# Kernel tuning notes

Measured on AMD Instinct MI355X. Metric: run time of the kernel, lower is better.

Reference implementation:

```python
import jax, jax.numpy as jnp
import numpy as np

B, P, T = 64, 49, 20      # batch, num_pixels (7x7), caption length
V, E, D, A, ENC = 32000, 512, 512, 512, 2048


def setup_inputs() -> dict:
    key = jax.random.key(0)
    ks = jax.random.split(key, 20)
    s = 0.02
    return {
        "features": jax.random.normal(ks[0], (B, P, ENC), jnp.float32),
        "captions": jax.random.randint(ks[1], (B, T), 0, V, jnp.int64),
        "embed_table": jax.random.normal(ks[2], (V, E), jnp.float32) * s,
        "W_ih": jax.random.normal(ks[3], (4 * D, ENC + E), jnp.float32) * s,
        "b_ih": jnp.zeros((4 * D,), jnp.float32),
        "W_hh": jax.random.normal(ks[4], (4 * D, D), jnp.float32) * s,
        "b_hh": jnp.zeros((4 * D,), jnp.float32),
        "W_init_h": jax.random.normal(ks[5], (ENC, D), jnp.float32) * s,
        "b_init_h": jnp.zeros((D,), jnp.float32),
        "W_init_c": jax.random.normal(ks[6], (ENC, D), jnp.float32) * s,
        "b_init_c": jnp.zeros((D,), jnp.float32),
        "W_enc_att": jax.random.normal(ks[7], (ENC, A), jnp.float32) * s,
        "b_enc_att": jnp.zeros((A,), jnp.float32),
        "W_dec_att": jax.random.normal(ks[8], (D, A), jnp.float32) * s,
        "b_dec_att": jnp.zeros((A,), jnp.float32),
        "w_A": jax.random.normal(ks[9], (A,), jnp.float32) * s,
        "b_A": jnp.zeros((), jnp.float32),
        "W_out": jax.random.normal(ks[10], (D, V), jnp.float32) * s,
        "b_out": jnp.zeros((V,), jnp.float32),
    }


def reference(features, captions, embed_table, W_ih, b_ih, W_hh, b_hh,
              W_init_h, b_init_h, W_init_c, b_init_c,
              W_enc_att, b_enc_att, W_dec_att, b_dec_att, w_A, b_A,
              W_out, b_out):
    # Dropout is treated as identity (eval mode) for a deterministic baseline.
    bsz, seq_len = captions.shape
    emb = embed_table[captions]                              # [B,T,E]
    mean_f = features.mean(axis=1)                           # [B,ENC]
    h0 = mean_f @ W_init_h + b_init_h                        # [B,D]
    c0 = mean_f @ W_init_c + b_init_c                        # [B,D]
    enc_states = features @ W_enc_att + b_enc_att            # [B,P,A] (precomputed, loop-invariant)

    def step(carry, x_t):
        h, c = carry
        dec = h @ W_dec_att + b_dec_att                      # [B,A]
        comb = jnp.tanh(enc_states + dec[:, None, :])        # [B,P,A]
        scores = comb @ w_A + b_A                            # [B,P]
        alpha = jax.nn.softmax(scores, axis=1)
        ctx = jnp.einsum('bpe,bp->be', features, alpha)      # [B,ENC]
        x = jnp.concatenate([ctx, x_t], axis=1)              # [B,ENC+E]
        gates = x @ W_ih.T + b_ih + h @ W_hh.T + b_hh        # [B,4D]
        i, f, g, o = jnp.split(gates, 4, axis=1)
        i, f, o = jax.nn.sigmoid(i), jax.nn.sigmoid(f), jax.nn.sigmoid(o)
        g = jnp.tanh(g)
        c2 = f * c + i * g
        h2 = o * jnp.tanh(c2)
        logits = h2 @ W_out + b_out                          # [B,V]
        return (h2, c2), logits

    xs = jnp.swapaxes(emb[:, :seq_len - 1], 0, 1)            # [T-1,B,E]
    _, preds = jax.lax.scan(step, (h0, c0), xs)              # [T-1,B,V]
    preds = jnp.swapaxes(preds, 0, 1)                        # [B,T-1,V]
    vocab = W_out.shape[1]
    last = jnp.zeros((bsz, 1, vocab), preds.dtype)           # t = T-1 never written
    return jnp.concatenate([preds, last], axis=1)            # [B,T,V]
```

## Files before the change

kernel.cpp:

```cpp
#include <hip/hip_runtime.h>

constexpr int B_   = 64;
constexpr int P_   = 49;
constexpr int T_   = 20;
constexpr int V_   = 32000;
constexpr int E_   = 512;
constexpr int D_   = 512;
constexpr int A_   = 512;
constexpr int ENC_ = 2048;
constexpr int NT_  = T_ - 1;
constexpr int KX_  = ENC_ + E_ + D_;
constexpr int KSPL = 8;
constexpr int GCH  = (KX_ / 64) / KSPL;

#define DI __device__ __forceinline__

using u16 = unsigned short;
typedef short   bf16x8 __attribute__((ext_vector_type(8)));
typedef float   f32x4  __attribute__((ext_vector_type(4)));
typedef u16     u16x4  __attribute__((ext_vector_type(4)));

DI float sigm(float x) { return 1.0f / (1.0f + __expf(-x)); }
DI float tanhx(float x) {
  x = fminf(15.0f, fmaxf(-15.0f, x));
  float e = __expf(2.0f * x);
  return (e - 1.0f) / (e + 1.0f);
}
DI u16 f2bf(float x) {
  union { float f; unsigned u; } v{x};
  unsigned r = v.u + 0x7FFF + ((v.u >> 16) & 1);
  return (u16)(r >> 16);
}
DI float bf2f(u16 x) {
  union { unsigned u; float f; } v;
  v.u = ((unsigned)x) << 16;
  return v.f;
}
DI f32x4 mfma16(bf16x8 a, bf16x8 b, f32x4 c) {
  return __builtin_amdgcn_mfma_f32_16x16x32_bf16(a, b, c, 0, 0, 0);
}


__global__ __launch_bounds__(256) void k_mean_bf(const float* __restrict__ feat,
                                                 u16* __restrict__ mfb) {
  int idx = blockIdx.x * 256 + threadIdx.x;
  int b = idx >> 11, e = idx & (ENC_ - 1);
  const float* f = feat + (size_t)b * P_ * ENC_ + e;
  float s = 0.f;
#pragma unroll
  for (int p = 0; p < P_; p++) s += f[(size_t)p * ENC_];
  mfb[idx] = f2bf(s * (1.0f / P_));
}

__global__ __launch_bounds__(256) void k_tr_cvt(const float* __restrict__ in,
    u16* __restrict__ outp, int R, int C) {
  __shared__ float tbuf[32][33];
  int tx = threadIdx.x & 31, ty = threadIdx.x >> 5;
  int c0 = blockIdx.x * 32, r0 = blockIdx.y * 32;
#pragma unroll
  for (int i = 0; i < 4; i++)
    tbuf[ty + 8 * i][tx] = in[(size_t)(r0 + ty + 8 * i) * C + c0 + tx];
  __syncthreads();
#pragma unroll
  for (int i = 0; i < 4; i++)
    outp[(size_t)(c0 + ty + 8 * i) * R + r0 + tx] = f2bf(tbuf[tx][ty + 8 * i]);
}

__global__ __launch_bounds__(256) void k_cvt4(const float* __restrict__ in,
                                              u16* __restrict__ o) {
  int i = blockIdx.x * 256 + threadIdx.x;
  float4 v = ((const float4*)in)[i];
  u16x4 r = {f2bf(v.x), f2bf(v.y), f2bf(v.z), f2bf(v.w)};
  ((u16x4*)o)[i] = r;
}

__global__ __launch_bounds__(256) void k_wg4(const float* __restrict__ Wih,
    const float* __restrict__ Whh, u16* __restrict__ Wg) {
  int i = blockIdx.x * 256 + threadIdx.x;
  int j = i / 768, rem = i - j * 768;
  int k = rem * 4;
  const float* src = (k < ENC_ + E_) ? (Wih + (size_t)j * (ENC_ + E_) + k)
                                     : (Whh + (size_t)j * D_ + (k - ENC_ - E_));
  float4 v = *(const float4*)src;
  u16x4 r = {f2bf(v.x), f2bf(v.y), f2bf(v.z), f2bf(v.w)};
  ((u16x4*)Wg)[i] = r;
}

__global__ __launch_bounds__(256) void k_emb_bf(const int* __restrict__ cap,
    const float* __restrict__ tab, u16* __restrict__ embb) {
  int idx = blockIdx.x * 256 + threadIdx.x;
  int e = idx & (E_ - 1);
  int tb = idx >> 9;
  int b = tb & 63, t = tb >> 6;
  embb[idx] = f2bf(tab[(size_t)cap[b * T_ + t] * E_ + e]);
}

__global__ __launch_bounds__(256) void k_init_bf(const u16* __restrict__ mfb,
    const u16* __restrict__ WiT, const float* __restrict__ binh,
    const float* __restrict__ binc, u16* __restrict__ hbf, float* __restrict__ c) {
  int wid = threadIdx.x >> 6, lane = threadIdx.x & 63;
  int n0 = blockIdx.x * 64 + wid * 16;
  int l16 = lane & 15, lk = lane >> 4;
  const u16* bp = WiT + (size_t)(n0 + l16) * ENC_ + 8 * lk;
  const u16* ap = mfb + (size_t)l16 * ENC_ + 8 * lk;
  f32x4 acc[4] = {};
#pragma unroll 4
  for (int kc = 0; kc < ENC_; kc += 32) {
    bf16x8 b = *(const bf16x8*)(bp + kc);
#pragma unroll
    for (int mf = 0; mf < 4; mf++) {
      bf16x8 a = *(const bf16x8*)(ap + (size_t)mf * 16 * ENC_ + kc);
      acc[mf] = mfma16(a, b, acc[mf]);
    }
  }
  int n = n0 + l16;
#pragma unroll
  for (int mf = 0; mf < 4; mf++) {
    int m = mf * 16 + 4 * lk;
#pragma unroll
    for (int r = 0; r < 4; r++) {
      float v = acc[mf][r];
      if (n < D_) hbf[(size_t)(m + r) * D_ + n] = f2bf(v + binh[n]);
      else        c[(size_t)(m + r) * D_ + (n - D_)] = v + binc[n - D_];
    }
  }
}


__global__ __launch_bounds__(256) void k_enc_bf(const u16* __restrict__ fb,
    const u16* __restrict__ WeT, const float* __restrict__ benc,
    float* __restrict__ encs) {
  int wid = threadIdx.x >> 6, lane = threadIdx.x & 63;
  int m0 = blockIdx.x * 64, n0 = blockIdx.y * 64 + wid * 16;
  int l16 = lane & 15, lk = lane >> 4;
  const u16* ap = fb + (size_t)(m0 + l16) * ENC_ + 8 * lk;
  const u16* bp = WeT + (size_t)(n0 + l16) * ENC_ + 8 * lk;
  f32x4 acc[4] = {};
#pragma unroll 8
  for (int i = 0; i < ENC_ / 32; i++) {
    int kc = i * 32;
    bf16x8 b = *(const bf16x8*)(bp + kc);
#pragma unroll
    for (int mf = 0; mf < 4; mf++) {
      bf16x8 a = *(const bf16x8*)(ap + (size_t)mf * 16 * ENC_ + kc);
      acc[mf] = mfma16(a, b, acc[mf]);
    }
  }
  float bv = benc[n0 + l16];
#pragma unroll
  for (int mf = 0; mf < 4; mf++) {
    int m = m0 + mf * 16 + 4 * lk;
#pragma unroll
    for (int r = 0; r < 4; r++)
      encs[(size_t)(m + r) * A_ + n0 + l16] = acc[mf][r] + bv;
  }
}

__global__ __launch_bounds__(256) void k_gates_bf(const u16* __restrict__ ctxb,
    const u16* __restrict__ embb, const u16* __restrict__ hbf,
    const u16* __restrict__ Wg, float* __restrict__ gp, int t) {
  int wid = threadIdx.x >> 6, lane = threadIdx.x & 63;
  int j0 = blockIdx.x * 64 + wid * 16;
  int sp = blockIdx.y;
  int l16 = lane & 15, lk = lane >> 4;
  const u16* bp = Wg + (size_t)(j0 + l16) * KX_ + 8 * lk;
  f32x4 acc[4] = {};
#pragma unroll
  for (int i = 0; i < KX_ / KSPL / 32; i++) {
    int kc = sp * (KX_ / KSPL) + i * 32;
    int k = kc + 8 * lk;
    bf16x8 b = *(const bf16x8*)(bp + kc);
#pragma unroll
    for (int mf = 0; mf < 4; mf++) {
      int row = mf * 16 + l16;
      const u16* src;
      if (k < ENC_)            src = ctxb + (size_t)row * ENC_ + k;
      else if (k < ENC_ + E_)  src = embb + ((size_t)t * B_ + row) * E_ + (k - ENC_);
      else                     src = hbf + (size_t)row * D_ + (k - ENC_ - E_);
      bf16x8 a = *(const bf16x8*)src;
      acc[mf] = mfma16(a, b, acc[mf]);
    }
  }
#pragma unroll
  for (int mf = 0; mf < 4; mf++) {
    int m = mf * 16 + 4 * lk;
#pragma unroll
    for (int r = 0; r < 4; r++)
      gp[((size_t)sp * B_ + m + r) * (4 * D_) + j0 + l16] = acc[mf][r];
  }
}

__global__ __launch_bounds__(256) void k_logits_all2(const u16* __restrict__ hall,
    const u16* __restrict__ WoT, const float* __restrict__ bout,
    float* __restrict__ out) {
  int wid = threadIdx.x >> 6, lane = threadIdx.x & 63;
  int n0 = blockIdx.x * 64 + wid * 16;
  int l16 = lane & 15, lk = lane >> 4;
  bf16x8 bfr[16];
  const u16* bp = WoT + (size_t)(n0 + l16) * D_ + 8 * lk;
#pragma unroll
  for (int kc = 0; kc < 16; kc++) bfr[kc] = *(const bf16x8*)(bp + kc * 32);
  float bv = bout[n0 + l16];
#pragma unroll 1
  for (int s = 0; s < NT_; s++) {
    const u16* ap = hall + (size_t)s * B_ * D_ + (size_t)l16 * D_ + 8 * lk;
    f32x4 acc[4] = {};
#pragma unroll
    for (int kc = 0; kc < 16; kc++) {
#pragma unroll
      for (int mf = 0; mf < 4; mf++) {
        bf16x8 a = *(const bf16x8*)(ap + (size_t)mf * 16 * D_ + kc * 32);
        acc[mf] = mfma16(a, bfr[kc], acc[mf]);
      }
    }
#pragma unroll
    for (int mf = 0; mf < 4; mf++) {
      int m = mf * 16 + 4 * lk;
#pragma unroll
      for (int r = 0; r < 4; r++)
        out[((size_t)(m + r) * T_ + s) * V_ + n0 + l16] = acc[mf][r] + bv;
    }
  }
#pragma unroll
  for (int mf = 0; mf < 4; mf++) {
    int m = mf * 16 + 4 * lk;
#pragma unroll
    for (int r = 0; r < 4; r++)
      out[((size_t)(m + r) * T_ + (T_ - 1)) * V_ + n0 + l16] = 0.f;
  }
}


__global__ __launch_bounds__(512) void k_att3(const u16* __restrict__ featb,
    const float* __restrict__ encs, const u16* __restrict__ WdT,
    const float* __restrict__ bdec, const float* __restrict__ wA,
    const float* __restrict__ bA, const float* __restrict__ gp,
    const float* __restrict__ bih, const float* __restrict__ bhh,
    const float* __restrict__ c_in, float* __restrict__ c_out,
    u16* __restrict__ hbf, u16* __restrict__ hallp, u16* __restrict__ ctxb,
    int do_reduce, int do_att) {
  __shared__ u16 hsb[D_];
  __shared__ float ds[A_];
  __shared__ float sc[P_];
  __shared__ float inv_s;
  int b = blockIdx.x, y = blockIdx.y, tid = threadIdx.x;

  if (do_reduce) {
    int d = tid;
    float g0 = 0, g1 = 0, g2 = 0, g3 = 0;
#pragma unroll
    for (int s = 0; s < KSPL; s++) {
      const float* g = gp + (size_t)(s * B_ + b) * (4 * D_);
      g0 += g[d]; g1 += g[D_ + d]; g2 += g[2 * D_ + d]; g3 += g[3 * D_ + d];
    }
    g0 += bih[d] + bhh[d];
    g1 += bih[D_ + d] + bhh[D_ + d];
    g2 += bih[2 * D_ + d] + bhh[2 * D_ + d];
    g3 += bih[3 * D_ + d] + bhh[3 * D_ + d];
    float iv = sigm(g0), fv = sigm(g1), gv = tanhx(g2), ov = sigm(g3);
    float cv = fmaf(fv, c_in[b * D_ + d], iv * gv);
    float hv = ov * tanhx(cv);
    u16 hb = f2bf(hv);
    hsb[d] = hb;
    if (y == 0) {
      c_out[b * D_ + d] = cv;
      hbf[b * D_ + d] = hb;
      hallp[b * D_ + d] = hb;
    }
  } else {
    hsb[tid] = hbf[b * D_ + tid];
  }
  __syncthreads();
  if (!do_att) return;

  {
    int w = tid >> 6, lane = tid & 63, l16 = lane & 15, lk = lane >> 4;
#pragma unroll
    for (int f = 0; f < 4; f++) {
      int n = w * 64 + f * 16 + l16;
      const u16* bp = WdT + (size_t)n * D_ + 8 * lk;
      f32x4 acc = {};
#pragma unroll
      for (int kc = 0; kc < D_; kc += 32) {
        bf16x8 av = *(const bf16x8*)(hsb + kc + 8 * lk);
        bf16x8 bv = *(const bf16x8*)(bp + kc);
        acc = mfma16(av, bv, acc);
      }
      if (lk == 0) ds[n] = acc[0] + bdec[n];
    }
  }
  __syncthreads();

  int wv_ = tid >> 6, ln = tid & 63;
  float bA0 = bA[0];
  for (int p = wv_; p < P_; p += 8) {
    const float* ep = encs + (size_t)(b * P_ + p) * A_;
    float s = 0.f;
#pragma unroll
    for (int a = ln; a < A_; a += 64) s += tanhx(ep[a] + ds[a]) * wA[a];
#pragma unroll
    for (int off = 32; off; off >>= 1) s += __shfl_down(s, off);
    if (ln == 0) sc[p] = s + bA0;
  }
  __syncthreads();

  if (tid == 0) {
    float mx = -1e30f;
    for (int p = 0; p < P_; p++) mx = fmaxf(mx, sc[p]);
    float sum = 0.f;
    for (int p = 0; p < P_; p++) { float ex = __expf(sc[p] - mx); sc[p] = ex; sum += ex; }
    inv_s = 1.0f / sum;
  }
  __syncthreads();

  float inv = inv_s;
#pragma unroll
  for (int q = 0; q < 2; q++) {
    int e = y * 1024 + q * 512 + tid;
    const u16* fp = featb + (size_t)b * P_ * ENC_ + e;
    float s = 0.f;
#pragma unroll
    for (int p = 0; p < P_; p++) s = fmaf(bf2f(fp[(size_t)p * ENC_]), sc[p], s);
    ctxb[b * ENC_ + e] = f2bf(s * inv);
  }
}


DI int swz(int row, int slot) { return row * 64 + ((slot ^ (row >> 2)) << 2); }

__global__ __launch_bounds__(256) void k_mean(const float* __restrict__ feat,
                                              float* __restrict__ mf) {
  int idx = blockIdx.x * 256 + threadIdx.x;
  int b = idx >> 11, e = idx & (ENC_ - 1);
  const float* f = feat + (size_t)b * P_ * ENC_ + e;
  float s = 0.f;
#pragma unroll
  for (int p = 0; p < P_; p++) s += f[(size_t)p * ENC_];
  mf[idx] = s * (1.0f / P_);
}

__global__ __launch_bounds__(256) void k_emb(const int* __restrict__ cap,
                                             const float* __restrict__ tab,
                                             float* __restrict__ emb) {
  int idx = blockIdx.x * 256 + threadIdx.x;
  int e  = idx & (E_ - 1);
  int bt = idx >> 9;
  int b = bt / NT_, t = bt - b * NT_;
  int tok = cap[b * T_ + t];
  emb[idx] = tab[(size_t)tok * E_ + e];
}

__global__ __launch_bounds__(256) void k_init(const float* __restrict__ mf,
    const float* __restrict__ Wh, const float* __restrict__ bh,
    const float* __restrict__ Wc, const float* __restrict__ bc,
    float* __restrict__ h, float* __restrict__ c) {
  __shared__ float ms[ENC_];
  int b = blockIdx.y;
  for (int i = threadIdx.x; i < ENC_; i += 256) ms[i] = mf[b * ENC_ + i];
  __syncthreads();
  int d = blockIdx.x * 256 + threadIdx.x;
  const float* W = blockIdx.z ? Wc : Wh;
  float s = (blockIdx.z ? bc : bh)[d];
#pragma unroll 8
  for (int e = 0; e < ENC_; e++) s = fmaf(ms[e], W[(size_t)e * D_ + d], s);
  (blockIdx.z ? c : h)[b * D_ + d] = s;
}

__global__ __launch_bounds__(256) void k_zero_last(float* __restrict__ out) {
  int i = blockIdx.x * 256 + threadIdx.x;
  int b = i / 8000, v4 = i - b * 8000;
  float4 z = {0.f, 0.f, 0.f, 0.f};
  *(float4*)(out + ((size_t)b * T_ + (T_ - 1)) * V_ + (size_t)v4 * 4) = z;
}

__global__ __launch_bounds__(256) void k_enc(const float* __restrict__ Ag,
    const float* __restrict__ Wg, const float* __restrict__ bias,
    float* __restrict__ Cg) {
  __shared__ float As[64 * 64], Ws[64 * 64];
  int m0 = blockIdx.x * 64, n0 = blockIdx.y * 64;
  int tid = threadIdx.x, tn = tid & 15, tm = tid >> 4;
  float acc[4][4] = {};
#pragma unroll 1
  for (int ch = 0; ch < ENC_ / 64; ch++) {
    int k0 = ch * 64;
    __syncthreads();
#pragma unroll
    for (int q = 0; q < 4; q++) {
      int idx = tid + q * 256;
      int row = idx >> 4, slot = idx & 15;
      *(float4*)&As[swz(row, slot)] =
          *(const float4*)(Ag + (size_t)(m0 + row) * ENC_ + k0 + slot * 4);
      *(float4*)&Ws[swz(row, slot)] =
          *(const float4*)(Wg + (size_t)(k0 + row) * A_ + n0 + slot * 4);
    }
    __syncthreads();
#pragma unroll
    for (int kk = 0; kk < 16; kk++) {
      float4 av[4], wv[4];
#pragma unroll
      for (int i = 0; i < 4; i++) av[i] = *(float4*)&As[swz(4 * tm + i, kk)];
#pragma unroll
      for (int u = 0; u < 4; u++) wv[u] = *(float4*)&Ws[swz(4 * kk + u, tn)];
      const float* wq = (const float*)wv;
#pragma unroll
      for (int i = 0; i < 4; i++) {
        const float* aq = (const float*)&av[i];
#pragma unroll
        for (int j = 0; j < 4; j++) {
          float s = acc[i][j];
#pragma unroll
          for (int u = 0; u < 4; u++) s = fmaf(aq[u], wq[u * 4 + j], s);
          acc[i][j] = s;
        }
      }
    }
  }
#pragma unroll
  for (int i = 0; i < 4; i++) {
    int m = m0 + 4 * tm + i, n = n0 + 4 * tn;
    float4 bv = *(const float4*)(bias + n);
    float4 o = {acc[i][0] + bv.x, acc[i][1] + bv.y, acc[i][2] + bv.z, acc[i][3] + bv.w};
    *(float4*)(Cg + (size_t)m * A_ + n) = o;
  }
}

__global__ __launch_bounds__(256) void k_logits(const float* __restrict__ h,
    const float* __restrict__ Wout, const float* __restrict__ bout,
    float* __restrict__ out, int t) {
  __shared__ float As[64 * 64], Ws[64 * 64];
  int n0 = blockIdx.x * 64;
  int tid = threadIdx.x, tn = tid & 15, tm = tid >> 4;
  float acc[4][4] = {};
#pragma unroll 1
  for (int ch = 0; ch < D_ / 64; ch++) {
    int k0 = ch * 64;
    __syncthreads();
#pragma unroll
    for (int q = 0; q < 4; q++) {
      int idx = tid + q * 256;
      int row = idx >> 4, slot = idx & 15;
      *(float4*)&As[swz(row, slot)] =
          *(const float4*)(h + (size_t)row * D_ + k0 + slot * 4);
      *(float4*)&Ws[swz(row, slot)] =
          *(const float4*)(Wout + (size_t)(k0 + row) * V_ + n0 + slot * 4);
    }
    __syncthreads();
#pragma unroll
    for (int kk = 0; kk < 16; kk++) {
      float4 av[4], wv[4];
#pragma unroll
      for (int i = 0; i < 4; i++) av[i] = *(float4*)&As[swz(4 * tm + i, kk)];
#pragma unroll
      for (int u = 0; u < 4; u++) wv[u] = *(float4*)&Ws[swz(4 * kk + u, tn)];
      const float* wq = (const float*)wv;
#pragma unroll
      for (int i = 0; i < 4; i++) {
        const float* aq = (const float*)&av[i];
#pragma unroll
        for (int j = 0; j < 4; j++) {
          float s = acc[i][j];
#pragma unroll
          for (int u = 0; u < 4; u++) s = fmaf(aq[u], wq[u * 4 + j], s);
          acc[i][j] = s;
        }
      }
    }
  }
#pragma unroll
  for (int i = 0; i < 4; i++) {
    int m = 4 * tm + i, n = n0 + 4 * tn;
    float4 bv = *(const float4*)(bout + n);
    float4 o = {acc[i][0] + bv.x, acc[i][1] + bv.y, acc[i][2] + bv.z, acc[i][3] + bv.w};
    *(float4*)(out + ((size_t)m * T_ + t) * V_ + n) = o;
  }
}

__global__ __launch_bounds__(256) void k_gates(const float* __restrict__ ctx,
    const float* __restrict__ emb, const float* __restrict__ h,
    const float* __restrict__ Wih, const float* __restrict__ Whh,
    float* __restrict__ gp, int t) {
  __shared__ float As[64 * 64], Ws[64 * 64];
  int n0 = blockIdx.x * 64;
  int sp = blockIdx.y;
  int tid = threadIdx.x, tn = tid & 15, tm = tid >> 4;
  float acc[4][4] = {};
#pragma unroll 1
  for (int ch = 0; ch < GCH; ch++) {
    int k0 = sp * (GCH * 64) + ch * 64;
    __syncthreads();
#pragma unroll
    for (int q = 0; q < 4; q++) {
      int idx = tid + q * 256;
      int row = idx >> 4, slot = idx & 15;
      int k = k0 + slot * 4;
      float4 xv;
      if (k < ENC_)            xv = *(const float4*)(ctx + (size_t)row * ENC_ + k);
      else if (k < ENC_ + E_)  xv = *(const float4*)(emb + ((size_t)row * NT_ + t) * E_ + (k - ENC_));
      else                     xv = *(const float4*)(h + (size_t)row * D_ + (k - ENC_ - E_));
      *(float4*)&As[swz(row, slot)] = xv;
      int j = n0 + row;
      float4 wv2;
      if (k < ENC_ + E_) wv2 = *(const float4*)(Wih + (size_t)j * (ENC_ + E_) + k);
      else               wv2 = *(const float4*)(Whh + (size_t)j * D_ + (k - ENC_ - E_));
      *(float4*)&Ws[swz(row, slot)] = wv2;
    }
    __syncthreads();
#pragma unroll
    for (int kk = 0; kk < 16; kk++) {
      float4 av[4], wv[4];
#pragma unroll
      for (int i = 0; i < 4; i++) av[i] = *(float4*)&As[swz(4 * tm + i, kk)];
#pragma unroll
      for (int j = 0; j < 4; j++) wv[j] = *(float4*)&Ws[swz(4 * tn + j, kk)];
#pragma unroll
      for (int i = 0; i < 4; i++) {
        const float* aq = (const float*)&av[i];
#pragma unroll
        for (int j = 0; j < 4; j++) {
          const float* wqj = (const float*)&wv[j];
          float s = acc[i][j];
#pragma unroll
          for (int u = 0; u < 4; u++) s = fmaf(aq[u], wqj[u], s);
          acc[i][j] = s;
        }
      }
    }
  }
#pragma unroll
  for (int i = 0; i < 4; i++) {
    int b = 4 * tm + i, j = n0 + 4 * tn;
    float4 o = {acc[i][0], acc[i][1], acc[i][2], acc[i][3]};
    *(float4*)(gp + ((size_t)(sp * B_ + b)) * (4 * D_) + j) = o;
  }
}

__global__ __launch_bounds__(512) void k_att(const float* __restrict__ feat,
    const float* __restrict__ encs, const float* __restrict__ Wdec,
    const float* __restrict__ bdec, const float* __restrict__ wA,
    const float* __restrict__ bA, const float* __restrict__ gp,
    const float* __restrict__ bih, const float* __restrict__ bhh,
    float* __restrict__ h, float* __restrict__ c, float* __restrict__ ctx,
    int do_reduce, int do_att) {
  __shared__ float hs[D_];
  __shared__ float ds[A_];
  __shared__ float sc[P_];
  __shared__ float inv_s;
  int b = blockIdx.x, tid = threadIdx.x;

  if (do_reduce) {
    int d = tid;
    float g0 = 0, g1 = 0, g2 = 0, g3 = 0;
#pragma unroll
    for (int s = 0; s < KSPL; s++) {
      const float* g = gp + (size_t)(s * B_ + b) * (4 * D_);
      g0 += g[d]; g1 += g[D_ + d]; g2 += g[2 * D_ + d]; g3 += g[3 * D_ + d];
    }
    g0 += bih[d] + bhh[d];
    g1 += bih[D_ + d] + bhh[D_ + d];
    g2 += bih[2 * D_ + d] + bhh[2 * D_ + d];
    g3 += bih[3 * D_ + d] + bhh[3 * D_ + d];
    float iv = sigm(g0), fv = sigm(g1), gv = tanhx(g2), ov = sigm(g3);
    float cv = fmaf(fv, c[b * D_ + d], iv * gv);
    float hv = ov * tanhx(cv);
    c[b * D_ + d] = cv;
    h[b * D_ + d] = hv;
    hs[d] = hv;
  } else {
    hs[tid] = h[b * D_ + tid];
  }
  __syncthreads();
  if (!do_att) return;

  {
    int a = tid;
    float s = bdec[a];
#pragma unroll 8
    for (int d = 0; d < D_; d++) s = fmaf(hs[d], Wdec[(size_t)d * A_ + a], s);
    ds[a] = s;
  }
  __syncthreads();

  int wv_ = tid >> 6, ln = tid & 63;
  float bA0 = bA[0];
  for (int p = wv_; p < P_; p += 8) {
    const float* ep = encs + (size_t)(b * P_ + p) * A_;
    float s = 0.f;
#pragma unroll
    for (int a = ln; a < A_; a += 64) s += tanhx(ep[a] + ds[a]) * wA[a];
#pragma unroll
    for (int off = 32; off; off >>= 1) s += __shfl_down(s, off);
    if (ln == 0) sc[p] = s + bA0;
  }
  __syncthreads();

  if (tid == 0) {
    float mx = -1e30f;
    for (int p = 0; p < P_; p++) mx = fmaxf(mx, sc[p]);
    float sum = 0.f;
    for (int p = 0; p < P_; p++) { float ex = __expf(sc[p] - mx); sc[p] = ex; sum += ex; }
    inv_s = 1.0f / sum;
  }
  __syncthreads();

  float inv = inv_s;
  for (int e = tid; e < ENC_; e += 512) {
    const float* fp = feat + (size_t)b * P_ * ENC_ + e;
    float s = 0.f;
#pragma unroll
    for (int p = 0; p < P_; p++) s = fmaf(fp[(size_t)p * ENC_], sc[p], s);
    ctx[b * ENC_ + e] = s * inv;
  }
}


extern "C" void kernel_launch(void* const* d_in, const int* in_sizes, int n_in,
                              void* d_out, int out_size, void* d_ws, size_t ws_size,
                              hipStream_t stream) {
  const float* features = (const float*)d_in[0];
  const int*   captions = (const int*)d_in[1];
  const float* table    = (const float*)d_in[2];
  const float* Wih  = (const float*)d_in[3];
  const float* bih  = (const float*)d_in[4];
  const float* Whh  = (const float*)d_in[5];
  const float* bhh  = (const float*)d_in[6];
  const float* Winh = (const float*)d_in[7];
  const float* binh = (const float*)d_in[8];
  const float* Winc = (const float*)d_in[9];
  const float* binc = (const float*)d_in[10];
  const float* Wenc = (const float*)d_in[11];
  const float* benc = (const float*)d_in[12];
  const float* Wdec = (const float*)d_in[13];
  const float* bdec = (const float*)d_in[14];
  const float* wA   = (const float*)d_in[15];
  const float* bA   = (const float*)d_in[16];
  const float* Wout = (const float*)d_in[17];
  const float* bout = (const float*)d_in[18];
  float* out = (float*)d_out;

  constexpr size_t F_ENC = (size_t)B_ * P_ * A_;
  constexpr size_t F_C   = (size_t)B_ * D_;
  constexpr size_t F_GP  = (size_t)KSPL * B_ * 4 * D_;
  constexpr size_t U_WOT = (size_t)V_ * D_;
  constexpr size_t U_WG  = (size_t)(4 * D_) * KX_;
  constexpr size_t U_HBF = (size_t)B_ * D_;
  constexpr size_t U_CTX = (size_t)B_ * ENC_;
  constexpr size_t U_FEAT = (size_t)B_ * P_ * ENC_;
  constexpr size_t U_WET = (size_t)A_ * ENC_;
  constexpr size_t U_EMB = (size_t)NT_ * B_ * E_;
  constexpr size_t U_WDT = (size_t)A_ * D_;
  constexpr size_t U_HALL = (size_t)NT_ * B_ * D_;
  static_assert(U_EMB + U_WDT <= U_WET, "embb+WdT overlay WeT region");
  constexpr size_t NEED_BYTES =
      (F_ENC + 2 * F_C + F_GP) * 4 +
      (U_WOT + U_WG + U_HBF + U_CTX + U_FEAT + U_WET + U_HALL) * 2;

  if (ws_size >= NEED_BYTES) {
    float* ws = (float*)d_ws;
    float* enc_states = ws;
    float* cbuf0  = enc_states + F_ENC;
    float* cbuf1  = cbuf0 + F_C;
    float* gparts = cbuf1 + F_C;
    u16* WoT   = (u16*)(gparts + F_GP);
    u16* Wg    = WoT + U_WOT;
    u16* hbf   = Wg + U_WG;
    u16* ctxb  = hbf + U_HBF;
    u16* featb = ctxb + U_CTX;
    u16* wetr  = featb + U_FEAT;
    u16* WeT   = wetr;
    u16* embb  = wetr;
    u16* WdT   = wetr + U_EMB;
    u16* hall  = wetr + U_WET;
    u16* WiT   = (u16*)gparts;
    u16* mfb   = ctxb;
    float* cb[2] = {cbuf0, cbuf1};

    k_mean_bf<<<512, 256, 0, stream>>>(features, mfb);
    k_tr_cvt<<<dim3(D_ / 32, ENC_ / 32), 256, 0, stream>>>(Winh, WiT, ENC_, D_);
    k_tr_cvt<<<dim3(D_ / 32, ENC_ / 32), 256, 0, stream>>>(Winc, WiT + (size_t)D_ * ENC_, ENC_, D_);
    k_init_bf<<<16, 256, 0, stream>>>(mfb, WiT, binh, binc, hbf, cbuf0);
    k_cvt4<<<(int)(U_FEAT / 4 / 256), 256, 0, stream>>>(features, featb);
    k_tr_cvt<<<dim3(A_ / 32, ENC_ / 32), 256, 0, stream>>>(Wenc, WeT, ENC_, A_);
    k_enc_bf<<<dim3(49, 8), 256, 0, stream>>>(featb, WeT, benc, enc_states);
    k_emb_bf<<<2432, 256, 0, stream>>>(captions, table, embb);
    k_tr_cvt<<<dim3(A_ / 32, D_ / 32), 256, 0, stream>>>(Wdec, WdT, D_, A_);
    k_tr_cvt<<<dim3(V_ / 32, D_ / 32), 256, 0, stream>>>(Wout, WoT, D_, V_);
    k_wg4<<<(int)(U_WG / 4 / 256), 256, 0, stream>>>(Wih, Whh, Wg);

    for (int t = 0; t < NT_; t++) {
      u16* hallp = (t > 0) ? (hall + (size_t)(t - 1) * B_ * D_) : hall;
      const float* cin = cb[(t > 0 ? (t - 1) : 0) & 1];
      float* cout = cb[t & 1];
      k_att3<<<dim3(64, 2), 512, 0, stream>>>(featb, enc_states, WdT, bdec, wA,
                                              bA, gparts, bih, bhh, cin, cout,
                                              hbf, hallp, ctxb, t > 0 ? 1 : 0, 1);
      k_gates_bf<<<dim3(32, KSPL), 256, 0, stream>>>(ctxb, embb, hbf, Wg, gparts, t);
    }
    k_att3<<<dim3(64, 1), 512, 0, stream>>>(featb, enc_states, WdT, bdec, wA,
                                            bA, gparts, bih, bhh,
                                            cb[(NT_ - 1) & 1], cb[NT_ & 1], hbf,
                                            hall + (size_t)(NT_ - 1) * B_ * D_,
                                            ctxb, 1, 0);
    k_logits_all2<<<500, 256, 0, stream>>>(hall, WoT, bout, out);
  } else {
    float* ws = (float*)d_ws;
    float* enc_states = ws;
    float* mean_f = enc_states + (size_t)B_ * P_ * A_;
    float* emb    = mean_f + (size_t)B_ * ENC_;
    float* h      = emb + (size_t)B_ * NT_ * E_;
    float* c      = h + (size_t)B_ * D_;
    float* ctx    = c + (size_t)B_ * D_;
    float* gparts = ctx + (size_t)B_ * ENC_;

    k_mean<<<512, 256, 0, stream>>>(features, mean_f);
    k_emb<<<2432, 256, 0, stream>>>(captions, table, emb);
    k_init<<<dim3(2, 64, 2), 256, 0, stream>>>(mean_f, Winh, binh, Winc, binc, h, c);
    k_enc<<<dim3(49, 8), 256, 0, stream>>>(features, Wenc, benc, enc_states);
    k_zero_last<<<2000, 256, 0, stream>>>(out);

    for (int t = 0; t < NT_; t++) {
      k_att<<<64, 512, 0, stream>>>(features, enc_states, Wdec, bdec, wA, bA,
                                    gparts, bih, bhh, h, c, ctx, t > 0 ? 1 : 0, 1);
      if (t > 0)
        k_logits<<<500, 256, 0, stream>>>(h, Wout, bout, out, t - 1);
      k_gates<<<dim3(32, KSPL), 256, 0, stream>>>(ctx, emb, h, Wih, Whh, gparts, t);
    }
    k_att<<<64, 512, 0, stream>>>(features, enc_states, Wdec, bdec, wA, bA,
                                  gparts, bih, bhh, h, c, ctx, 1, 0);
    k_logits<<<500, 256, 0, stream>>>(h, Wout, bout, out, NT_ - 1);
  }
}
```

Baseline: 1.264 ms.

## Fuse prologue kernels, per-step embedding gather, and restructure logits GEMM

Merges the many prologue conversion and transpose kernels into one multi-role launch, and merges the init and encoder-projection GEMMs into a second. The per-step attention kernel now gathers that step's embedding, and gate K-splits drop from 8 to 4. The attention grid is no longer split across ctx halves, so each block computes the full context with vectorized loads. The logits kernel is retiled to keep h fragments in registers and stage outputs in shared memory for coalesced float4 stores. This cuts launch count and improves store coalescing, at the cost of less parallelism per step and a very large shared buffer in the fused prologue.

```diff
diff --git a/kernel.cpp b/kernel.cpp
--- a/kernel.cpp
+++ b/kernel.cpp
@@ -12,6 +12,7 @@
 constexpr int KX_  = ENC_ + E_ + D_;
 constexpr int KSPL = 8;
 constexpr int GCH  = (KX_ / 64) / KSPL;
+constexpr int KS4  = 4;
 
 #define DI __device__ __forceinline__
 
@@ -40,23 +41,13 @@
   return __builtin_amdgcn_mfma_f32_16x16x32_bf16(a, b, c, 0, 0, 0);
 }
 
-
-__global__ __launch_bounds__(256) void k_mean_bf(const float* __restrict__ feat,
-                                                 u16* __restrict__ mfb) {
-  int idx = blockIdx.x * 256 + threadIdx.x;
-  int b = idx >> 11, e = idx & (ENC_ - 1);
-  const float* f = feat + (size_t)b * P_ * ENC_ + e;
-  float s = 0.f;
-#pragma unroll
-  for (int p = 0; p < P_; p++) s += f[(size_t)p * ENC_];
-  mfb[idx] = f2bf(s * (1.0f / P_));
-}
-
-__global__ __launch_bounds__(256) void k_tr_cvt(const float* __restrict__ in,
-    u16* __restrict__ outp, int R, int C) {
-  __shared__ float tbuf[32][33];
+constexpr int PRO1_BLOCKS = 18756;
+
+DI void dev_tr_cvt(const float* in, u16* outp, int R, int C, int bx, int by,
+                   char* smem) {
+  float (*tbuf)[33] = (float(*)[33])smem;
   int tx = threadIdx.x & 31, ty = threadIdx.x >> 5;
-  int c0 = blockIdx.x * 32, r0 = blockIdx.y * 32;
+  int c0 = bx * 32, r0 = by * 32;
 #pragma unroll
   for (int i = 0; i < 4; i++)
     tbuf[ty + 8 * i][tx] = in[(size_t)(r0 + ty + 8 * i) * C + c0 + tx];
@@ -66,99 +57,249 @@
     outp[(size_t)(c0 + ty + 8 * i) * R + r0 + tx] = f2bf(tbuf[tx][ty + 8 * i]);
 }
 
-__global__ __launch_bounds__(256) void k_cvt4(const float* __restrict__ in,
-                                              u16* __restrict__ o) {
-  int i = blockIdx.x * 256 + threadIdx.x;
-  float4 v = ((const float4*)in)[i];
-  u16x4 r = {f2bf(v.x), f2bf(v.y), f2bf(v.z), f2bf(v.w)};
-  ((u16x4*)o)[i] = r;
-}
-
-__global__ __launch_bounds__(256) void k_wg4(const float* __restrict__ Wih,
-    const float* __restrict__ Whh, u16* __restrict__ Wg) {
-  int i = blockIdx.x * 256 + threadIdx.x;
-  int j = i / 768, rem = i - j * 768;
-  int k = rem * 4;
-  const float* src = (k < ENC_ + E_) ? (Wih + (size_t)j * (ENC_ + E_) + k)
-                                     : (Whh + (size_t)j * D_ + (k - ENC_ - E_));
-  float4 v = *(const float4*)src;
-  u16x4 r = {f2bf(v.x), f2bf(v.y), f2bf(v.z), f2bf(v.w)};
-  ((u16x4*)Wg)[i] = r;
-}
-
-__global__ __launch_bounds__(256) void k_emb_bf(const int* __restrict__ cap,
-    const float* __restrict__ tab, u16* __restrict__ embb) {
-  int idx = blockIdx.x * 256 + threadIdx.x;
-  int e = idx & (E_ - 1);
-  int tb = idx >> 9;
-  int b = tb & 63, t = tb >> 6;
-  embb[idx] = f2bf(tab[(size_t)cap[b * T_ + t] * E_ + e]);
-}
-
-__global__ __launch_bounds__(256) void k_init_bf(const u16* __restrict__ mfb,
+__global__ __launch_bounds__(256) void k_pro1(
+    const float* __restrict__ feat, const float* __restrict__ Winh,
+    const float* __restrict__ Winc, const float* __restrict__ Wenc,
+    const float* __restrict__ Wdec, const float* __restrict__ Wout,
+    const float* __restrict__ Wih, const float* __restrict__ Whh,
+    float* __restrict__ out, u16* __restrict__ mfb, u16* __restrict__ featb,
+    u16* __restrict__ WiT, u16* __restrict__ WeT, u16* __restrict__ WdT,
+    u16* __restrict__ WoT, u16* __restrict__ Wg) {
+  __shared__ __align__(16) char smem[67584];
+  int bid = blockIdx.x;
+  if (bid < 2000) {
+    int i = bid * 256 + threadIdx.x;
+    int b = i / 8000, v4 = i - b * 8000;
+    float4 z = {0.f, 0.f, 0.f, 0.f};
+    *(float4*)(out + ((size_t)b * T_ + (T_ - 1)) * V_ + (size_t)v4 * 4) = z;
+  } else if (bid < 8272) {
+    int i = (bid - 2000) * 256 + threadIdx.x;
+    float4 v = ((const float4*)feat)[i];
+    u16x4 r = {f2bf(v.x), f2bf(v.y), f2bf(v.z), f2bf(v.w)};
+    ((u16x4*)featb)[i] = r;
+  } else if (bid < 8784) {
+    int idx = (bid - 8272) * 256 + threadIdx.x;
+    int b = idx >> 11, e = idx & (ENC_ - 1);
+    const float* f = feat + (size_t)b * P_ * ENC_ + e;
+    float s = 0.f;
+#pragma unroll
+    for (int p = 0; p < P_; p++) s += f[(size_t)p * ENC_];
+    mfb[idx] = f2bf(s * (1.0f / P_));
+  } else if (bid < 9808) {
+    int l = bid - 8784;
+    dev_tr_cvt(Winh, WiT, ENC_, D_, l & 15, l >> 4, smem);
+  } else if (bid < 10832) {
+    int l = bid - 9808;
+    dev_tr_cvt(Winc, WiT + (size_t)D_ * ENC_, ENC_, D_, l & 15, l >> 4, smem);
+  } else if (bid < 11856) {
+    int l = bid - 10832;
+    dev_tr_cvt(Wenc, WeT, ENC_, A_, l & 15, l >> 4, smem);
+  } else if (bid < 12112) {
+    int l = bid - 11856;
+    dev_tr_cvt(Wdec, WdT, D_, A_, l & 15, l >> 4, smem);
+  } else if (bid < 12612) {
+    int l = bid - 12112;
+    int bx = l % 250, by = l / 250;
+    u16 (*ld)[264] = (u16(*)[264])smem;
+    int v0 = bx * 128, k0 = by * 256;
+    int vf = (threadIdx.x & 31) * 4, kk = threadIdx.x >> 5;
+#pragma unroll 4
+    for (int p = 0; p < 32; p++) {
+      int k = kk + p * 8;
+      float4 v = *(const float4*)(Wout + (size_t)(k0 + k) * V_ + v0 + vf);
+      ld[vf + 0][k] = f2bf(v.x);
+      ld[vf + 1][k] = f2bf(v.y);
+      ld[vf + 2][k] = f2bf(v.z);
+      ld[vf + 3][k] = f2bf(v.w);
+    }
+    __syncthreads();
+    int v = threadIdx.x >> 1, h = threadIdx.x & 1;
+    u16* op = WoT + (size_t)(v0 + v) * D_ + k0 + h * 128;
+#pragma unroll
+    for (int i = 0; i < 16; i++)
+      *(bf16x8*)(op + i * 8) = *(const bf16x8*)(&ld[v][h * 128 + i * 8]);
+  } else {
+    int i = (bid - 12612) * 256 + threadIdx.x;
+    int j = i / 768, rem = i - j * 768;
+    int k = rem * 4;
+    const float* src = (k < ENC_ + E_) ? (Wih + (size_t)j * (ENC_ + E_) + k)
+                                       : (Whh + (size_t)j * D_ + (k - ENC_ - E_));
+    float4 v = *(const float4*)src;
+    u16x4 r = {f2bf(v.x), f2bf(v.y), f2bf(v.z), f2bf(v.w)};
+    ((u16x4*)Wg)[i] = r;
+  }
+}
+
+
+__global__ __launch_bounds__(256) void k_pro2(const u16* __restrict__ mfb,
     const u16* __restrict__ WiT, const float* __restrict__ binh,
-    const float* __restrict__ binc, u16* __restrict__ hbf, float* __restrict__ c) {
-  int wid = threadIdx.x >> 6, lane = threadIdx.x & 63;
-  int n0 = blockIdx.x * 64 + wid * 16;
-  int l16 = lane & 15, lk = lane >> 4;
-  const u16* bp = WiT + (size_t)(n0 + l16) * ENC_ + 8 * lk;
-  const u16* ap = mfb + (size_t)l16 * ENC_ + 8 * lk;
-  f32x4 acc[4] = {};
-#pragma unroll 4
-  for (int kc = 0; kc < ENC_; kc += 32) {
-    bf16x8 b = *(const bf16x8*)(bp + kc);
-#pragma unroll
-    for (int mf = 0; mf < 4; mf++) {
-      bf16x8 a = *(const bf16x8*)(ap + (size_t)mf * 16 * ENC_ + kc);
-      acc[mf] = mfma16(a, b, acc[mf]);
-    }
-  }
-  int n = n0 + l16;
-#pragma unroll
-  for (int mf = 0; mf < 4; mf++) {
-    int m = mf * 16 + 4 * lk;
-#pragma unroll
-    for (int r = 0; r < 4; r++) {
-      float v = acc[mf][r];
-      if (n < D_) hbf[(size_t)(m + r) * D_ + n] = f2bf(v + binh[n]);
-      else        c[(size_t)(m + r) * D_ + (n - D_)] = v + binc[n - D_];
-    }
-  }
-}
-
-
-__global__ __launch_bounds__(256) void k_enc_bf(const u16* __restrict__ fb,
+    const float* __restrict__ binc, u16* __restrict__ hbf,
+    float* __restrict__ c, const u16* __restrict__ featb,
     const u16* __restrict__ WeT, const float* __restrict__ benc,
     float* __restrict__ encs) {
   int wid = threadIdx.x >> 6, lane = threadIdx.x & 63;
-  int m0 = blockIdx.x * 64, n0 = blockIdx.y * 64 + wid * 16;
   int l16 = lane & 15, lk = lane >> 4;
-  const u16* ap = fb + (size_t)(m0 + l16) * ENC_ + 8 * lk;
-  const u16* bp = WeT + (size_t)(n0 + l16) * ENC_ + 8 * lk;
-  f32x4 acc[4] = {};
+  if (blockIdx.x < 16) {
+    int n0 = blockIdx.x * 64 + wid * 16;
+    const u16* bp = WiT + (size_t)(n0 + l16) * ENC_ + 8 * lk;
+    const u16* ap = mfb + (size_t)l16 * ENC_ + 8 * lk;
+    f32x4 acc[4] = {};
+#pragma unroll 4
+    for (int kc = 0; kc < ENC_; kc += 32) {
+      bf16x8 b = *(const bf16x8*)(bp + kc);
+#pragma unroll
+      for (int mf = 0; mf < 4; mf++) {
+        bf16x8 a = *(const bf16x8*)(ap + (size_t)mf * 16 * ENC_ + kc);
+        acc[mf] = mfma16(a, b, acc[mf]);
+      }
+    }
+    int n = n0 + l16;
+#pragma unroll
+    for (int mf = 0; mf < 4; mf++) {
+      int m = mf * 16 + 4 * lk;
+#pragma unroll
+      for (int r = 0; r < 4; r++) {
+        float v = acc[mf][r];
+        if (n < D_) hbf[(size_t)(m + r) * D_ + n] = f2bf(v + binh[n]);
+        else        c[(size_t)(m + r) * D_ + (n - D_)] = v + binc[n - D_];
+      }
+    }
+  } else {
+    int l = blockIdx.x - 16;
+    int m0 = (l % 49) * 64, n0 = (l / 49) * 64 + wid * 16;
+    const u16* ap = featb + (size_t)(m0 + l16) * ENC_ + 8 * lk;
+    const u16* bp = WeT + (size_t)(n0 + l16) * ENC_ + 8 * lk;
+    f32x4 acc[4] = {};
 #pragma unroll 8
-  for (int i = 0; i < ENC_ / 32; i++) {
-    int kc = i * 32;
-    bf16x8 b = *(const bf16x8*)(bp + kc);
+    for (int i = 0; i < ENC_ / 32; i++) {
+      int kc = i * 32;
+      bf16x8 b = *(const bf16x8*)(bp + kc);
+#pragma unroll
+      for (int mf = 0; mf < 4; mf++) {
+        bf16x8 a = *(const bf16x8*)(ap + (size_t)mf * 16 * ENC_ + kc);
+        acc[mf] = mfma16(a, b, acc[mf]);
+      }
+    }
+    float bv = benc[n0 + l16];
 #pragma unroll
     for (int mf = 0; mf < 4; mf++) {
-      bf16x8 a = *(const bf16x8*)(ap + (size_t)mf * 16 * ENC_ + kc);
-      acc[mf] = mfma16(a, b, acc[mf]);
-    }
-  }
-  float bv = benc[n0 + l16];
-#pragma unroll
-  for (int mf = 0; mf < 4; mf++) {
-    int m = m0 + mf * 16 + 4 * lk;
-#pragma unroll
-    for (int r = 0; r < 4; r++)
-      encs[(size_t)(m + r) * A_ + n0 + l16] = acc[mf][r] + bv;
-  }
-}
-
-__global__ __launch_bounds__(256) void k_gates_bf(const u16* __restrict__ ctxb,
-    const u16* __restrict__ embb, const u16* __restrict__ hbf,
-    const u16* __restrict__ Wg, float* __restrict__ gp, int t) {
+      int m = m0 + mf * 16 + 4 * lk;
+#pragma unroll
+      for (int r = 0; r < 4; r++)
+        encs[(size_t)(m + r) * A_ + n0 + l16] = acc[mf][r] + bv;
+    }
+  }
+}
+
+
+__global__ __launch_bounds__(512) void k_att5(const u16* __restrict__ featb,
+    const float* __restrict__ encs, const u16* __restrict__ WdT,
+    const float* __restrict__ bdec, const float* __restrict__ wA,
+    const float* __restrict__ bA, const float* __restrict__ gp,
+    const float* __restrict__ bih, const float* __restrict__ bhh,
+    float* __restrict__ c, u16* __restrict__ hbf, u16* __restrict__ hallp,
+    u16* __restrict__ ctxb, const int* __restrict__ cap,
+    const float* __restrict__ tab, u16* __restrict__ embt, int t,
+    int do_reduce, int do_att) {
+  __shared__ u16 hsb[D_];
+  __shared__ float ds[A_];
+  __shared__ float sc[P_];
+  __shared__ float inv_s;
+  int b = blockIdx.x, tid = threadIdx.x;
+
+  if (do_att) {
+    int tok = cap[b * T_ + t];
+    embt[(size_t)b * E_ + tid] = f2bf(tab[(size_t)tok * E_ + tid]);
+  }
+
+  if (do_reduce) {
+    int d = tid;
+    float g0 = 0, g1 = 0, g2 = 0, g3 = 0;
+#pragma unroll
+    for (int s = 0; s < KS4; s++) {
+      const float* g = gp + (size_t)(s * B_ + b) * (4 * D_);
+      g0 += g[d]; g1 += g[D_ + d]; g2 += g[2 * D_ + d]; g3 += g[3 * D_ + d];
+    }
+    g0 += bih[d] + bhh[d];
+    g1 += bih[D_ + d] + bhh[D_ + d];
+    g2 += bih[2 * D_ + d] + bhh[2 * D_ + d];
+    g3 += bih[3 * D_ + d] + bhh[3 * D_ + d];
+    float iv = sigm(g0), fv = sigm(g1), gv = tanhx(g2), ov = sigm(g3);
+    float cv = fmaf(fv, c[b * D_ + d], iv * gv);
+    float hv = ov * tanhx(cv);
+    c[b * D_ + d] = cv;
+    u16 hb = f2bf(hv);
+    hsb[d] = hb;
+    hbf[b * D_ + d] = hb;
+    hallp[b * D_ + d] = hb;
+  } else {
+    hsb[tid] = hbf[b * D_ + tid];
+  }
+  __syncthreads();
+  if (!do_att) return;
+
+  {
+    int w = tid >> 6, lane = tid & 63, l16 = lane & 15, lk = lane >> 4;
+#pragma unroll
+    for (int f = 0; f < 4; f++) {
+      int n = w * 64 + f * 16 + l16;
+      const u16* bp = WdT + (size_t)n * D_ + 8 * lk;
+      f32x4 acc = {};
+#pragma unroll
+      for (int kc = 0; kc < D_; kc += 32) {
+        bf16x8 av = *(const bf16x8*)(hsb + kc + 8 * lk);
+        bf16x8 bv = *(const bf16x8*)(bp + kc);
+        acc = mfma16(av, bv, acc);
+      }
+      if (lk == 0) ds[n] = acc[0] + bdec[n];
+    }
+  }
+  __syncthreads();
+
+  {
+    int wv_ = tid >> 6, ln = tid & 63;
+    float bA0 = bA[0];
+    for (int p = wv_; p < P_; p += 8) {
+      const float* ep = encs + (size_t)(b * P_ + p) * A_;
+      float s = 0.f;
+#pragma unroll
+      for (int a = ln; a < A_; a += 64) s += tanhx(ep[a] + ds[a]) * wA[a];
+#pragma unroll
+      for (int off = 32; off; off >>= 1) s += __shfl_down(s, off);
+      if (ln == 0) sc[p] = s + bA0;
+    }
+  }
+  __syncthreads();
+  if (tid == 0) {
+    float mx = -1e30f;
+    for (int p = 0; p < P_; p++) mx = fmaxf(mx, sc[p]);
+    float sum = 0.f;
+    for (int p = 0; p < P_; p++) { float ex = __expf(sc[p] - mx); sc[p] = ex; sum += ex; }
+    inv_s = 1.0f / sum;
+  }
+  __syncthreads();
+  {
+    float inv = inv_s;
+    int e = tid * 4;
+    const u16* fp = featb + (size_t)b * P_ * ENC_ + e;
+    float s0 = 0.f, s1 = 0.f, s2 = 0.f, s3 = 0.f;
+#pragma unroll
+    for (int p = 0; p < P_; p++) {
+      u16x4 w = *(const u16x4*)(fp + (size_t)p * ENC_);
+      float scp = sc[p];
+      s0 = fmaf(bf2f(w.x), scp, s0);
+      s1 = fmaf(bf2f(w.y), scp, s1);
+      s2 = fmaf(bf2f(w.z), scp, s2);
+      s3 = fmaf(bf2f(w.w), scp, s3);
+    }
+    u16x4 o = {f2bf(s0 * inv), f2bf(s1 * inv), f2bf(s2 * inv), f2bf(s3 * inv)};
+    *(u16x4*)(ctxb + b * ENC_ + e) = o;
+  }
+}
+
+__global__ __launch_bounds__(256) void k_gates4(const u16* __restrict__ ctxb,
+    const u16* __restrict__ embt, const u16* __restrict__ hbf,
+    const u16* __restrict__ Wg, float* __restrict__ gp) {
   int wid = threadIdx.x >> 6, lane = threadIdx.x & 63;
   int j0 = blockIdx.x * 64 + wid * 16;
   int sp = blockIdx.y;
@@ -166,8 +307,8 @@
   const u16* bp = Wg + (size_t)(j0 + l16) * KX_ + 8 * lk;
   f32x4 acc[4] = {};
 #pragma unroll
-  for (int i = 0; i < KX_ / KSPL / 32; i++) {
-    int kc = sp * (KX_ / KSPL) + i * 32;
+  for (int i = 0; i < KX_ / KS4 / 32; i++) {
+    int kc = sp * (KX_ / KS4) + i * 32;
     int k = kc + 8 * lk;
     bf16x8 b = *(const bf16x8*)(bp + kc);
 #pragma unroll
@@ -175,7 +316,7 @@
       int row = mf * 16 + l16;
       const u16* src;
       if (k < ENC_)            src = ctxb + (size_t)row * ENC_ + k;
-      else if (k < ENC_ + E_)  src = embb + ((size_t)t * B_ + row) * E_ + (k - ENC_);
+      else if (k < ENC_ + E_)  src = embt + (size_t)row * E_ + (k - ENC_);
       else                     src = hbf + (size_t)row * D_ + (k - ENC_ - E_);
       bf16x8 a = *(const bf16x8*)src;
       acc[mf] = mfma16(a, b, acc[mf]);
@@ -190,138 +331,45 @@
   }
 }
 
-__global__ __launch_bounds__(256) void k_logits_all2(const u16* __restrict__ hall,
+
+__global__ __launch_bounds__(256) void k_logits5(const u16* __restrict__ hall,
     const u16* __restrict__ WoT, const float* __restrict__ bout,
     float* __restrict__ out) {
+  __shared__ float lt[16 * 1608];
+  int bid = blockIdx.x;
+  int vt = bid / 76;
+  int rem = bid - vt * 76;
+  int bg = rem / 19, s = rem - bg * 19;
+  int b0 = bg * 16;
   int wid = threadIdx.x >> 6, lane = threadIdx.x & 63;
-  int n0 = blockIdx.x * 64 + wid * 16;
   int l16 = lane & 15, lk = lane >> 4;
-  bf16x8 bfr[16];
-  const u16* bp = WoT + (size_t)(n0 + l16) * D_ + 8 * lk;
-#pragma unroll
-  for (int kc = 0; kc < 16; kc++) bfr[kc] = *(const bf16x8*)(bp + kc * 32);
-  float bv = bout[n0 + l16];
+
+  const u16* ap = hall + (size_t)s * B_ * D_ + (size_t)(b0 + l16) * D_ + 8 * lk;
+  bf16x8 afr[16];
+#pragma unroll
+  for (int kc = 0; kc < 16; kc++) afr[kc] = *(const bf16x8*)(ap + kc * 32);
+
 #pragma unroll 1
-  for (int s = 0; s < NT_; s++) {
-    const u16* ap = hall + (size_t)s * B_ * D_ + (size_t)l16 * D_ + 8 * lk;
-    f32x4 acc[4] = {};
-#pragma unroll
-    for (int kc = 0; kc < 16; kc++) {
-#pragma unroll
-      for (int mf = 0; mf < 4; mf++) {
-        bf16x8 a = *(const bf16x8*)(ap + (size_t)mf * 16 * D_ + kc * 32);
-        acc[mf] = mfma16(a, bfr[kc], acc[mf]);
-      }
-    }
-#pragma unroll
-    for (int mf = 0; mf < 4; mf++) {
-      int m = mf * 16 + 4 * lk;
-#pragma unroll
-      for (int r = 0; r < 4; r++)
-        out[((size_t)(m + r) * T_ + s) * V_ + n0 + l16] = acc[mf][r] + bv;
-    }
-  }
-#pragma unroll
-  for (int mf = 0; mf < 4; mf++) {
-    int m = mf * 16 + 4 * lk;
+  for (int tt = wid * 25; tt < (wid + 1) * 25; tt++) {
+    int col = vt * 1600 + tt * 16 + l16;
+    const u16* bp = WoT + (size_t)col * D_ + 8 * lk;
+    f32x4 acc = {};
+#pragma unroll
+    for (int kc = 0; kc < 16; kc++)
+      acc = mfma16(afr[kc], *(const bf16x8*)(bp + kc * 32), acc);
+    float bv = bout[col];
 #pragma unroll
     for (int r = 0; r < 4; r++)
-      out[((size_t)(m + r) * T_ + (T_ - 1)) * V_ + n0 + l16] = 0.f;
-  }
-}
-
-
-__global__ __launch_bounds__(512) void k_att3(const u16* __restrict__ featb,
-    const float* __restrict__ encs, const u16* __restrict__ WdT,
-    const float* __restrict__ bdec, const float* __restrict__ wA,
-    const float* __restrict__ bA, const float* __restrict__ gp,
-    const float* __restrict__ bih, const float* __restrict__ bhh,
-    const float* __restrict__ c_in, float* __restrict__ c_out,
-    u16* __restrict__ hbf, u16* __restrict__ hallp, u16* __restrict__ ctxb,
-    int do_reduce, int do_att) {
-  __shared__ u16 hsb[D_];
-  __shared__ float ds[A_];
-  __shared__ float sc[P_];
-  __shared__ float inv_s;
-  int b = blockIdx.x, y = blockIdx.y, tid = threadIdx.x;
-
-  if (do_reduce) {
-    int d = tid;
-    float g0 = 0, g1 = 0, g2 = 0, g3 = 0;
-#pragma unroll
-    for (int s = 0; s < KSPL; s++) {
-      const float* g = gp + (size_t)(s * B_ + b) * (4 * D_);
-      g0 += g[d]; g1 += g[D_ + d]; g2 += g[2 * D_ + d]; g3 += g[3 * D_ + d];
-    }
-    g0 += bih[d] + bhh[d];
-    g1 += bih[D_ + d] + bhh[D_ + d];
-    g2 += bih[2 * D_ + d] + bhh[2 * D_ + d];
-    g3 += bih[3 * D_ + d] + bhh[3 * D_ + d];
-    float iv = sigm(g0), fv = sigm(g1), gv = tanhx(g2), ov = sigm(g3);
-    float cv = fmaf(fv, c_in[b * D_ + d], iv * gv);
-    float hv = ov * tanhx(cv);
-    u16 hb = f2bf(hv);
-    hsb[d] = hb;
-    if (y == 0) {
-      c_out[b * D_ + d] = cv;
-      hbf[b * D_ + d] = hb;
-      hallp[b * D_ + d] = hb;
-    }
-  } else {
-    hsb[tid] = hbf[b * D_ + tid];
-  }
-  __syncthreads();
-  if (!do_att) return;
-
-  {
-    int w = tid >> 6, lane = tid & 63, l16 = lane & 15, lk = lane >> 4;
-#pragma unroll
-    for (int f = 0; f < 4; f++) {
-      int n = w * 64 + f * 16 + l16;
-      const u16* bp = WdT + (size_t)n * D_ + 8 * lk;
-      f32x4 acc = {};
-#pragma unroll
-      for (int kc = 0; kc < D_; kc += 32) {
-        bf16x8 av = *(const bf16x8*)(hsb + kc + 8 * lk);
-        bf16x8 bv = *(const bf16x8*)(bp + kc);
-        acc = mfma16(av, bv, acc);
-      }
-      if (lk == 0) ds[n] = acc[0] + bdec[n];
-    }
-  }
-  __syncthreads();
-
-  int wv_ = tid >> 6, ln = tid & 63;
-  float bA0 = bA[0];
-  for (int p = wv_; p < P_; p += 8) {
-    const float* ep = encs + (size_t)(b * P_ + p) * A_;
-    float s = 0.f;
-#pragma unroll
-    for (int a = ln; a < A_; a += 64) s += tanhx(ep[a] + ds[a]) * wA[a];
-#pragma unroll
-    for (int off = 32; off; off >>= 1) s += __shfl_down(s, off);
-    if (ln == 0) sc[p] = s + bA0;
-  }
-  __syncthreads();
-
-  if (tid == 0) {
-    float mx = -1e30f;
-    for (int p = 0; p < P_; p++) mx = fmaxf(mx, sc[p]);
-    float sum = 0.f;
-    for (int p = 0; p < P_; p++) { float ex = __expf(sc[p] - mx); sc[p] = ex; sum += ex; }
-    inv_s = 1.0f / sum;
-  }
-  __syncthreads();
-
-  float inv = inv_s;
-#pragma unroll
-  for (int q = 0; q < 2; q++) {
-    int e = y * 1024 + q * 512 + tid;
-    const u16* fp = featb + (size_t)b * P_ * ENC_ + e;
-    float s = 0.f;
-#pragma unroll
-    for (int p = 0; p < P_; p++) s = fmaf(bf2f(fp[(size_t)p * ENC_]), sc[p], s);
-    ctxb[b * ENC_ + e] = f2bf(s * inv);
+      lt[(4 * lk + r) * 1608 + tt * 16 + l16] = acc[r] + bv;
+  }
+  __syncthreads();
+  int r = threadIdx.x >> 4, c16 = threadIdx.x & 15;
+  float* op = out + ((size_t)(b0 + r) * T_ + s) * V_ + vt * 1600;
+  const float* lp = lt + r * 1608;
+#pragma unroll
+  for (int j = 0; j < 25; j++) {
+    int cc = (c16 + j * 16) * 4;
+    *(float4*)(op + cc) = *(const float4*)(lp + cc);
   }
 }
 
@@ -646,15 +694,16 @@
   constexpr size_t U_CTX = (size_t)B_ * ENC_;
   constexpr size_t U_FEAT = (size_t)B_ * P_ * ENC_;
   constexpr size_t U_WET = (size_t)A_ * ENC_;
-  constexpr size_t U_EMB = (size_t)NT_ * B_ * E_;
   constexpr size_t U_WDT = (size_t)A_ * D_;
   constexpr size_t U_HALL = (size_t)NT_ * B_ * D_;
-  static_assert(U_EMB + U_WDT <= U_WET, "embb+WdT overlay WeT region");
+  static_assert((size_t)KS4 * B_ * 4 * D_ <= F_GP, "gp(KS4) fits");
+  static_assert((size_t)B_ * E_ <= 2 * F_C, "embt fits in cbuf1");
   constexpr size_t NEED_BYTES =
       (F_ENC + 2 * F_C + F_GP) * 4 +
       (U_WOT + U_WG + U_HBF + U_CTX + U_FEAT + U_WET + U_HALL) * 2;
-
-  if (ws_size >= NEED_BYTES) {
+  constexpr size_t NEED2 = NEED_BYTES + U_WDT * 2;
+
+  if (ws_size >= NEED2) {
     float* ws = (float*)d_ws;
     float* enc_states = ws;
     float* cbuf0  = enc_states + F_ENC;
@@ -665,42 +714,32 @@
     u16* hbf   = Wg + U_WG;
     u16* ctxb  = hbf + U_HBF;
     u16* featb = ctxb + U_CTX;
-    u16* wetr  = featb + U_FEAT;
-    u16* WeT   = wetr;
-    u16* embb  = wetr;
-    u16* WdT   = wetr + U_EMB;
-    u16* hall  = wetr + U_WET;
+    u16* WeT   = featb + U_FEAT;
+    u16* hall  = WeT + U_WET;
+    u16* WdT   = hall + U_HALL;
     u16* WiT   = (u16*)gparts;
     u16* mfb   = ctxb;
-    float* cb[2] = {cbuf0, cbuf1};
-
-    k_mean_bf<<<512, 256, 0, stream>>>(features, mfb);
-    k_tr_cvt<<<dim3(D_ / 32, ENC_ / 32), 256, 0, stream>>>(Winh, WiT, ENC_, D_);
-    k_tr_cvt<<<dim3(D_ / 32, ENC_ / 32), 256, 0, stream>>>(Winc, WiT + (size_t)D_ * ENC_, ENC_, D_);
-    k_init_bf<<<16, 256, 0, stream>>>(mfb, WiT, binh, binc, hbf, cbuf0);
-    k_cvt4<<<(int)(U_FEAT / 4 / 256), 256, 0, stream>>>(features, featb);
-    k_tr_cvt<<<dim3(A_ / 32, ENC_ / 32), 256, 0, stream>>>(Wenc, WeT, ENC_, A_);
-    k_enc_bf<<<dim3(49, 8), 256, 0, stream>>>(featb, WeT, benc, enc_states);
-    k_emb_bf<<<2432, 256, 0, stream>>>(captions, table, embb);
-    k_tr_cvt<<<dim3(A_ / 32, D_ / 32), 256, 0, stream>>>(Wdec, WdT, D_, A_);
-    k_tr_cvt<<<dim3(V_ / 32, D_ / 32), 256, 0, stream>>>(Wout, WoT, D_, V_);
-    k_wg4<<<(int)(U_WG / 4 / 256), 256, 0, stream>>>(Wih, Whh, Wg);
+    u16* embt  = (u16*)cbuf1;
+
+    k_pro1<<<PRO1_BLOCKS, 256, 0, stream>>>(features, Winh, Winc, Wenc, Wdec,
+                                            Wout, Wih, Whh, out, mfb, featb,
+                                            WiT, WeT, WdT, WoT, Wg);
+    k_pro2<<<408, 256, 0, stream>>>(mfb, WiT, binh, binc, hbf, cbuf0, featb,
+                                    WeT, benc, enc_states);
 
     for (int t = 0; t < NT_; t++) {
       u16* hallp = (t > 0) ? (hall + (size_t)(t - 1) * B_ * D_) : hall;
-      const float* cin = cb[(t > 0 ? (t - 1) : 0) & 1];
-      float* cout = cb[t & 1];
-      k_att3<<<dim3(64, 2), 512, 0, stream>>>(featb, enc_states, WdT, bdec, wA,
-                                              bA, gparts, bih, bhh, cin, cout,
-                                              hbf, hallp, ctxb, t > 0 ? 1 : 0, 1);
-      k_gates_bf<<<dim3(32, KSPL), 256, 0, stream>>>(ctxb, embb, hbf, Wg, gparts, t);
-    }
-    k_att3<<<dim3(64, 1), 512, 0, stream>>>(featb, enc_states, WdT, bdec, wA,
-                                            bA, gparts, bih, bhh,
-                                            cb[(NT_ - 1) & 1], cb[NT_ & 1], hbf,
-                                            hall + (size_t)(NT_ - 1) * B_ * D_,
-                                            ctxb, 1, 0);
-    k_logits_all2<<<500, 256, 0, stream>>>(hall, WoT, bout, out);
+      k_att5<<<64, 512, 0, stream>>>(featb, enc_states, WdT, bdec, wA, bA,
+                                     gparts, bih, bhh, cbuf0, hbf, hallp, ctxb,
+                                     captions, table, embt, t,
+                                     t > 0 ? 1 : 0, 1);
+      k_gates4<<<dim3(32, KS4), 256, 0, stream>>>(ctxb, embt, hbf, Wg, gparts);
+    }
+    k_att5<<<64, 512, 0, stream>>>(featb, enc_states, WdT, bdec, wA, bA,
+                                   gparts, bih, bhh, cbuf0, hbf,
+                                   hall + (size_t)(NT_ - 1) * B_ * D_, ctxb,
+                                   captions, table, embt, 0, 1, 0);
+    k_logits5<<<20 * 4 * 19, 256, 0, stream>>>(hall, WoT, bout, out);
   } else {
     float* ws = (float*)d_ws;
     float* enc_states = ws;
```

Result: slower. 1.510 ms (+19.5%).
